# Performance work log

Measured on AMD Instinct MI355X. Metric: run time of the kernel, lower is better.

## Reference

```python
import jax, jax.numpy as jnp
import numpy as np

SCALING = 16.0 / 8.0  # lora_alpha / r


def setup_inputs() -> dict:
    key = jax.random.key(0)
    k1, k2, k3, k4 = jax.random.split(key, 4)
    V, D, R = 50257, 1024, 8
    B, S = 8, 2048
    x = jax.random.randint(k1, (B, S), 0, V, dtype=jnp.int32)
    W = jax.random.normal(k2, (V, D), dtype=jnp.float32)
    lora_A = jax.random.normal(k3, (R, V), dtype=jnp.float32)
    lora_B = jax.random.normal(k4, (D, R), dtype=jnp.float32)
    return {"x": x, "W": W, "lora_A": lora_A, "lora_B": lora_B}


def reference(x, W, lora_A, lora_B):
    # base embedding gather: [B, S, D]
    base = W[x]
    # Instead of materializing (lora_B @ lora_A).T [V, D], gather the needed
    # columns of lora_A per token and do a small r-dim matmul (same math).
    A_g = lora_A[:, x]  # [R, B, S]
    delta = jnp.einsum("dr,rbs->bsd", lora_B, A_g) * SCALING  # [B, S, D]
    return base + delta
```

## Files before the change

### kernel.cpp

```cpp
#include <hip/hip_runtime.h>


#define LORA_D 1024
#define LORA_R 8
#define BLOCK  256
#define TOKS_PER_BLOCK 8

typedef float v4f __attribute__((ext_vector_type(4)));

__global__ __launch_bounds__(BLOCK, 4) void lora_embed_kernel(
    const int*   __restrict__ x,
    const float* __restrict__ W,
    const float* __restrict__ lora_A,
    const float* __restrict__ lora_B,
    float*       __restrict__ out,
    int n_tokens, int V)
{
    const int tid = threadIdx.x;
    const int d0  = tid * 4;

    float b[4][LORA_R];
    #pragma unroll
    for (int j = 0; j < 4; ++j) {
        const v4f lo = *reinterpret_cast<const v4f*>(&lora_B[(size_t)(d0 + j) * LORA_R + 0]);
        const v4f hi = *reinterpret_cast<const v4f*>(&lora_B[(size_t)(d0 + j) * LORA_R + 4]);
        b[j][0] = 2.0f * lo.x; b[j][1] = 2.0f * lo.y;
        b[j][2] = 2.0f * lo.z; b[j][3] = 2.0f * lo.w;
        b[j][4] = 2.0f * hi.x; b[j][5] = 2.0f * hi.y;
        b[j][6] = 2.0f * hi.z; b[j][7] = 2.0f * hi.w;
    }

    const int tok0 = blockIdx.x * TOKS_PER_BLOCK;

    if (tok0 + TOKS_PER_BLOCK <= n_tokens) {
        int t[TOKS_PER_BLOCK];
        #pragma unroll
        for (int k = 0; k < TOKS_PER_BLOCK; ++k)
            t[k] = x[tok0 + k];

        v4f w[TOKS_PER_BLOCK];
        #pragma unroll
        for (int k = 0; k < TOKS_PER_BLOCK; ++k)
            w[k] = *reinterpret_cast<const v4f*>(&W[(size_t)t[k] * LORA_D + d0]);

        #pragma unroll
        for (int k = 0; k < TOKS_PER_BLOCK; ++k) {
            float a[LORA_R];
            #pragma unroll
            for (int r = 0; r < LORA_R; ++r)
                a[r] = lora_A[(size_t)r * V + t[k]];

            float acc[4] = {w[k].x, w[k].y, w[k].z, w[k].w};
            #pragma unroll
            for (int j = 0; j < 4; ++j)
                #pragma unroll
                for (int r = 0; r < LORA_R; ++r)
                    acc[j] = fmaf(b[j][r], a[r], acc[j]);

            v4f o; o.x = acc[0]; o.y = acc[1]; o.z = acc[2]; o.w = acc[3];
            __builtin_nontemporal_store(
                o, reinterpret_cast<v4f*>(&out[(size_t)(tok0 + k) * LORA_D + d0]));
        }
    } else {
        for (int tok = tok0; tok < n_tokens; ++tok) {
            const int t = x[tok];
            float a[LORA_R];
            #pragma unroll
            for (int r = 0; r < LORA_R; ++r)
                a[r] = lora_A[(size_t)r * V + t];
            const v4f w = *reinterpret_cast<const v4f*>(&W[(size_t)t * LORA_D + d0]);
            float acc[4] = {w.x, w.y, w.z, w.w};
            #pragma unroll
            for (int j = 0; j < 4; ++j)
                #pragma unroll
                for (int r = 0; r < LORA_R; ++r)
                    acc[j] = fmaf(b[j][r], a[r], acc[j]);
            v4f o; o.x = acc[0]; o.y = acc[1]; o.z = acc[2]; o.w = acc[3];
            *reinterpret_cast<v4f*>(&out[(size_t)tok * LORA_D + d0]) = o;
        }
    }
}

extern "C" void kernel_launch(void* const* d_in, const int* in_sizes, int n_in,
                              void* d_out, int out_size, void* d_ws, size_t ws_size,
                              hipStream_t stream) {
    const int*   x      = (const int*)  d_in[0];
    const float* W      = (const float*)d_in[1];
    const float* lora_A = (const float*)d_in[2];
    const float* lora_B = (const float*)d_in[3];
    float*       out    = (float*)d_out;

    const int n_tokens = in_sizes[0];
    const int V        = in_sizes[1] / LORA_D;

    const int grid = (n_tokens + TOKS_PER_BLOCK - 1) / TOKS_PER_BLOCK;
    lora_embed_kernel<<<grid, BLOCK, 0, stream>>>(x, W, lora_A, lora_B, out,
                                                  n_tokens, V);
}
```

Measured before the change: 28.47 us.

## Pre-transpose and pre-scale lora_A into workspace for contiguous per-token loads

Adds a pre-pass kernel that transposes lora_A from [R,V] to [V,R] in workspace and folds the scaling factor into it. The main kernel then loads each token's rank-8 vector with two vector loads instead of eight strided scalar loads spread across separate rows. The cost is an extra launch plus a full read and write of lora_A (about 1.6 MB each way) on every call, which may outweigh the saved strided gathers.

```diff
diff --git a/kernel.cpp b/kernel.cpp
--- a/kernel.cpp
+++ b/kernel.cpp
@@ -8,10 +8,21 @@
 
 typedef float v4f __attribute__((ext_vector_type(4)));
 
+__global__ void transpose_a_kernel(const float* __restrict__ lora_A,
+                                   float* __restrict__ At, int V)
+{
+    const int v = blockIdx.x * blockDim.x + threadIdx.x;
+    if (v < V) {
+        #pragma unroll
+        for (int r = 0; r < LORA_R; ++r)
+            At[(size_t)v * LORA_R + r] = 2.0f * lora_A[(size_t)r * V + v];
+    }
+}
+
 __global__ __launch_bounds__(BLOCK, 4) void lora_embed_kernel(
     const int*   __restrict__ x,
     const float* __restrict__ W,
-    const float* __restrict__ lora_A,
+    const float* __restrict__ At,
     const float* __restrict__ lora_B,
     float*       __restrict__ out,
     int n_tokens, int V)
@@ -24,10 +35,8 @@
     for (int j = 0; j < 4; ++j) {
         const v4f lo = *reinterpret_cast<const v4f*>(&lora_B[(size_t)(d0 + j) * LORA_R + 0]);
         const v4f hi = *reinterpret_cast<const v4f*>(&lora_B[(size_t)(d0 + j) * LORA_R + 4]);
-        b[j][0] = 2.0f * lo.x; b[j][1] = 2.0f * lo.y;
-        b[j][2] = 2.0f * lo.z; b[j][3] = 2.0f * lo.w;
-        b[j][4] = 2.0f * hi.x; b[j][5] = 2.0f * hi.y;
-        b[j][6] = 2.0f * hi.z; b[j][7] = 2.0f * hi.w;
+        b[j][0] = lo.x; b[j][1] = lo.y; b[j][2] = lo.z; b[j][3] = lo.w;
+        b[j][4] = hi.x; b[j][5] = hi.y; b[j][6] = hi.z; b[j][7] = hi.w;
     }
 
     const int tok0 = blockIdx.x * TOKS_PER_BLOCK;
@@ -45,10 +54,9 @@
 
         #pragma unroll
         for (int k = 0; k < TOKS_PER_BLOCK; ++k) {
-            float a[LORA_R];
-            #pragma unroll
-            for (int r = 0; r < LORA_R; ++r)
-                a[r] = lora_A[(size_t)r * V + t[k]];
+            const v4f a0 = *reinterpret_cast<const v4f*>(&At[(size_t)t[k] * LORA_R + 0]);
+            const v4f a1 = *reinterpret_cast<const v4f*>(&At[(size_t)t[k] * LORA_R + 4]);
+            const float a[LORA_R] = {a0.x, a0.y, a0.z, a0.w, a1.x, a1.y, a1.z, a1.w};
 
             float acc[4] = {w[k].x, w[k].y, w[k].z, w[k].w};
             #pragma unroll
@@ -64,10 +72,9 @@
     } else {
         for (int tok = tok0; tok < n_tokens; ++tok) {
             const int t = x[tok];
-            float a[LORA_R];
-            #pragma unroll
-            for (int r = 0; r < LORA_R; ++r)
-                a[r] = lora_A[(size_t)r * V + t];
+            const v4f a0 = *reinterpret_cast<const v4f*>(&At[(size_t)t * LORA_R + 0]);
+            const v4f a1 = *reinterpret_cast<const v4f*>(&At[(size_t)t * LORA_R + 4]);
+            const float a[LORA_R] = {a0.x, a0.y, a0.z, a0.w, a1.x, a1.y, a1.z, a1.w};
             const v4f w = *reinterpret_cast<const v4f*>(&W[(size_t)t * LORA_D + d0]);
             float acc[4] = {w.x, w.y, w.z, w.w};
             #pragma unroll
@@ -89,11 +96,15 @@
     const float* lora_A = (const float*)d_in[2];
     const float* lora_B = (const float*)d_in[3];
     float*       out    = (float*)d_out;
+    float*       At     = (float*)d_ws;
 
     const int n_tokens = in_sizes[0];
     const int V        = in_sizes[1] / LORA_D;
 
+    const int tgrid = (V + BLOCK - 1) / BLOCK;
+    transpose_a_kernel<<<tgrid, BLOCK, 0, stream>>>(lora_A, At, V);
+
     const int grid = (n_tokens + TOKS_PER_BLOCK - 1) / TOKS_PER_BLOCK;
-    lora_embed_kernel<<<grid, BLOCK, 0, stream>>>(x, W, lora_A, lora_B, out,
+    lora_embed_kernel<<<grid, BLOCK, 0, stream>>>(x, W, At, lora_B, out,
                                                   n_tokens, V);
 }
```

New measurement: 32.60 us. +14.5%, slower.
